# Kernel tuning notes

Measured on AMD Instinct MI355X. Metric: run time of the kernel, lower is better.

The kernel has to match this reference:

```python
import jax, jax.numpy as jnp
import numpy as np

G, P = 128, 32          # num scenes, peds per scene
H, E = 64, 64           # h_dim, embedding_dim_pooling
D1, D2 = 512, 1024      # mlp_pre_pool dims
EPS = 1e-5


def setup_inputs() -> dict:
    key = jax.random.key(0)
    ks = jax.random.split(key, 16)
    N = G * P
    starts = jnp.arange(G, dtype=jnp.int64) * P
    seq_start_end = jnp.stack([starts, starts + P], axis=1)
    def lin(k, fin, fout):
        kw, kb = jax.random.split(k)
        s = 1.0 / np.sqrt(fin)
        return (jax.random.uniform(kw, (fin, fout), jnp.float32, -s, s),
                jax.random.uniform(kb, (fout,), jnp.float32, -s, s))
    Ws, bs = lin(ks[0], 2, E)
    Wv, bv = lin(ks[1], 1, E)
    W1, b1 = lin(ks[2], 3 * E, D1)
    W2, b2 = lin(ks[3], D1, D2)
    return {
        "h_states": jax.random.normal(ks[4], (N, H), jnp.float32),
        "seq_start_end": seq_start_end,
        "end_pos": jax.random.normal(ks[5], (N, 2), jnp.float32),
        "end_pos_speed": jax.random.uniform(ks[6], (N, 1), jnp.float32),
        "Ws": Ws, "bs": bs, "Wv": Wv, "bv": bv,
        "W1": W1, "b1": b1, "g1": jnp.ones((D1,), jnp.float32), "be1": jnp.zeros((D1,), jnp.float32),
        "W2": W2, "b2": b2, "g2": jnp.ones((D2,), jnp.float32), "be2": jnp.zeros((D2,), jnp.float32),
    }


def _bn(h, gamma, beta):
    # BatchNorm1d in train mode, stats over the per-group edge batch (axes 1,2)
    m = h.mean(axis=(1, 2), keepdims=True)
    v = ((h - m) ** 2).mean(axis=(1, 2), keepdims=True)  # biased variance
    return (h - m) * jax.lax.rsqrt(v + EPS) * gamma + beta


def reference(h_states, seq_start_end, end_pos, end_pos_speed,
              Ws, bs, Wv, bv, W1, b1, g1, be1, W2, b2, g2, be2):
    g = seq_start_end.shape[0]
    p = h_states.shape[0] // g
    pos = end_pos.reshape(g, p, 2)
    spd = end_pos_speed.reshape(g, p, 1)
    hid = h_states.reshape(g, p, H)
    # edge (i, j): rel = pos[j] - pos[i]; features of j for hidden & speed
    rel = pos[:, None, :, :] - pos[:, :, None, :]          # [G,P(i),P(j),2]
    rel_e = rel @ Ws + bs                                   # [G,P,P,E]
    spd_e = spd @ Wv + bv                                   # [G,P,E]
    hid_b = jnp.broadcast_to(hid[:, None, :, :], (g, p, p, H))
    spd_b = jnp.broadcast_to(spd_e[:, None, :, :], (g, p, p, E))
    x = jnp.concatenate([rel_e, hid_b, spd_b], axis=-1)     # [G,P,P,3E]
    h1 = jax.nn.relu(_bn(x @ W1 + b1, g1, be1))             # [G,P,P,512]
    h2 = jax.nn.relu(_bn(h1 @ W2 + b2, g2, be2))            # [G,P,P,1024]
    pooled = h2.max(axis=2)                                 # max over j
    return pooled.reshape(g * p, -1)
```

## Files before the change

### kernel.cpp

```cpp
#include <hip/hip_runtime.h>
#include <cstdint>

typedef unsigned short ushort_t;
typedef __attribute__((ext_vector_type(8))) __bf16 bf16x8;
typedef __attribute__((ext_vector_type(4))) float f32x4;
typedef __attribute__((ext_vector_type(4))) int i32x4;

#define NG 128
#define NP 32
#define NH 64
#define ND1 512
#define ND2 1024

__device__ inline ushort_t f2bf(float f) {
    uint32_t u = __float_as_uint(f);
    uint32_t r = (u + 0x7FFFu + ((u >> 16) & 1u)) >> 16;
    return (ushort_t)r;
}

#define GLL16(gp, lp) __builtin_amdgcn_global_load_lds( \
    (const __attribute__((address_space(1))) unsigned int*)(gp), \
    (__attribute__((address_space(3))) unsigned int*)(lp), 16, 0, 0)

__global__ void k2_all(const float* __restrict__ hstates, const float* __restrict__ pos,
                       const float* __restrict__ spd, const float* __restrict__ W1,
                       const float* __restrict__ g1, const float* __restrict__ be1,
                       const float* __restrict__ Ws, const float* __restrict__ bs,
                       const float* __restrict__ Wv, const float* __restrict__ bv,
                       const float* __restrict__ b1, const float* __restrict__ W2,
                       ushort_t* __restrict__ W2T,
                       float* __restrict__ u1, float* __restrict__ w1,
                       float* __restrict__ psum) {
    __shared__ float hid_s[32][64];
    __shared__ float pos_s[32][2];
    __shared__ float spd_s[32];
    __shared__ ushort_t tile[64][65];
    int b = blockIdx.x, tid = threadIdx.x;
    if (b < 256) {
        int t0 = b * 256 + tid;
        #pragma unroll
        for (int z = 0; z < 4; z++) psum[t0 + z * 65536] = 0.f;
        int g = b >> 1;
        int ch = ((b & 1) << 8) + tid;
        for (int t = tid; t < 2048; t += 256) hid_s[t >> 6][t & 63] = hstates[g * 2048 + t];
        if (tid < 64) pos_s[tid >> 1][tid & 1] = pos[g * 64 + tid];
        if (tid < 32) spd_s[tid] = spd[g * 32 + tid];
        float m0 = 0.f, m1 = 0.f, uu = 0.f, vv = b1[ch];
        for (int e = 0; e < 64; e++) {
            float w1a = W1[e * ND1 + ch];
            float w1c = W1[(128 + e) * ND1 + ch];
            m0 += Ws[e] * w1a;
            m1 += Ws[64 + e] * w1a;
            uu += Wv[e] * w1c;
            vv += bs[e] * w1a + bv[e] * w1c;
        }
        __syncthreads();
        float cj[32], qj[32];
        #pragma unroll
        for (int j = 0; j < 32; j++) {
            qj[j] = pos_s[j][0] * m0 + pos_s[j][1] * m1;
            cj[j] = vv + spd_s[j] * uu;
        }
        for (int h = 0; h < 64; h++) {
            float w = W1[(64 + h) * ND1 + ch];
            #pragma unroll
            for (int j = 0; j < 32; j++) cj[j] += hid_s[j][h] * w;
        }
        float S1 = 0.f, S2 = 0.f, C1 = 0.f, Cq = 0.f, C2 = 0.f;
        #pragma unroll
        for (int j = 0; j < 32; j++) {
            S1 += qj[j]; S2 += qj[j] * qj[j];
            C1 += cj[j]; Cq += cj[j] * qj[j]; C2 += cj[j] * cj[j];
        }
        float mean = C1 * (1.0f / 32.0f);
        float sumsq = 64.f * S2 - 2.f * S1 * S1 + 64.f * Cq - 2.f * S1 * C1 + 32.f * C2;
        float var = sumsq * (1.0f / 1024.0f) - mean * mean;
        float A1 = rsqrtf(var + 1e-5f) * g1[ch];
        float B1 = be1[ch] - mean * A1;
        #pragma unroll
        for (int j = 0; j < 32; j++) {
            u1[(g * 32 + j) * ND1 + ch] = (qj[j] + cj[j]) * A1 + B1;
            w1[(g * 32 + j) * ND1 + ch] = qj[j] * A1;
        }
    } else {
        int tb = b - 256;
        int kb2 = tb & 7, nb = tb >> 3;
        #pragma unroll
        for (int e = 0; e < 16; e++) {
            int lin = tid + e * 256;
            int k = lin >> 6, n = lin & 63;
            tile[k][n] = f2bf(W2[(kb2 * 64 + k) * ND2 + nb * 64 + n]);
        }
        __syncthreads();
        #pragma unroll
        for (int e = 0; e < 16; e++) {
            int lin = tid + e * 256;
            int kl = lin & 63, nl = lin >> 6;
            int n = nb * 64 + nl, k = kb2 * 64 + kl;
            int idx = n * ND1 + ((k >> 6) << 6) + (((((k >> 3) & 7) ^ (n & 7))) << 3) + (k & 7);
            W2T[idx] = tile[kl][nl];
        }
    }
}

__global__ void k2b_h1(const float* __restrict__ u1c, const float* __restrict__ w1c,
                       ushort_t* __restrict__ h1) {
    int t = blockIdx.x * 256 + threadIdx.x;
    int k8 = t & 63;
    int row = t >> 6;
    int gc = row >> 10, rem = row & 1023;
    int i = rem >> 5, j = rem & 31;
    const float4* pu = reinterpret_cast<const float4*>(u1c + (size_t)(gc * 32 + j) * ND1 + k8 * 8);
    const float4* pw = reinterpret_cast<const float4*>(w1c + (size_t)(gc * 32 + i) * ND1 + k8 * 8);
    float4 ua = pu[0], ub = pu[1], wa = pw[0], wb = pw[1];
    uint32_t p0 = (uint32_t)f2bf(fmaxf(ua.x - wa.x, 0.f)) | ((uint32_t)f2bf(fmaxf(ua.y - wa.y, 0.f)) << 16);
    uint32_t p1 = (uint32_t)f2bf(fmaxf(ua.z - wa.z, 0.f)) | ((uint32_t)f2bf(fmaxf(ua.w - wa.w, 0.f)) << 16);
    uint32_t p2 = (uint32_t)f2bf(fmaxf(ub.x - wb.x, 0.f)) | ((uint32_t)f2bf(fmaxf(ub.y - wb.y, 0.f)) << 16);
    uint32_t p3 = (uint32_t)f2bf(fmaxf(ub.z - wb.z, 0.f)) | ((uint32_t)f2bf(fmaxf(ub.w - wb.w, 0.f)) << 16);
    i32x4 v = {(int)p0, (int)p1, (int)p2, (int)p3};
    int kt = k8 >> 3, c = k8 & 7;
    *reinterpret_cast<i32x4*>(h1 + (size_t)row * ND1 + (kt << 6) + (((c ^ (row & 7))) << 3)) = v;
}

#define BARX() do { __builtin_amdgcn_sched_barrier(0); __builtin_amdgcn_s_barrier(); __builtin_amdgcn_sched_barrier(0); } while (0)
#define STG(XG, XL, kt, h) do { \
    const char* _g = (XG) + (size_t)(h) * 131072 + (size_t)(kt) * 128; \
    char* _l = (XL) + (((kt) & 1) << 15) + ((h) << 14) + ldsw; \
    GLL16(_g, _l); \
    GLL16(_g + 65536, _l + 8192); \
} while (0)

__global__ __launch_bounds__(512, 2) void k3_gemm(
        const ushort_t* __restrict__ h1, const ushort_t* __restrict__ W2T,
        float* __restrict__ maxv, float* __restrict__ minv,
        float* __restrict__ psum, float* __restrict__ psq, int g0, int nwg8) {
    __shared__ __align__(16) char lds[131072];
    int b = blockIdx.x;
    int orig = (b & 7) * nwg8 + (b >> 3);
    int mt = orig >> 2, nt = orig & 3;
    int tid = threadIdx.x;
    int w = tid >> 6, l = tid & 63;
    int wm = w >> 2, wn = w & 3;
    int lo = l & 15, lhi = l >> 4;

    int srow = w * 8 + (l >> 3);
    int sbyte = (l & 7) * 16;
    const char* Agb = reinterpret_cast<const char*>(h1) + (size_t)(mt * 256 + srow) * 1024 + sbyte;
    const char* Bgb = reinterpret_cast<const char*>(W2T) + (size_t)(nt * 256 + srow) * 1024 + sbyte;
    char* ldsA = lds;
    char* ldsB = lds + 65536;
    int ldsw = w * 1024;

    int csw0 = ((lhi) ^ (lo & 7)) << 4;
    int csw1 = ((4 + lhi) ^ (lo & 7)) << 4;
    const char* aRB = ldsA + wm * 16384 + lo * 128;
    const char* bRB = ldsB + (wn >> 1) * 16384 + ((wn & 1) * 64 + lo) * 128;

    f32x4 acc[8][4];
    #pragma unroll
    for (int x = 0; x < 8; x++)
        #pragma unroll
        for (int y = 0; y < 4; y++) acc[x][y] = (f32x4){0.f, 0.f, 0.f, 0.f};

    bf16x8 a0[4][2], a1[4][2], bb0[2][2], bb1[2][2];

    auto rdA = [&](bf16x8 (&ar)[4][2], int slot, int qm) {
        #pragma unroll
        for (int f = 0; f < 4; f++) {
            ar[f][0] = *reinterpret_cast<const bf16x8*>(aRB + slot * 32768 + (qm * 64 + f * 16) * 128 + csw0);
            ar[f][1] = *reinterpret_cast<const bf16x8*>(aRB + slot * 32768 + (qm * 64 + f * 16) * 128 + csw1);
        }
    };
    auto rdB = [&](bf16x8 (&br)[2][2], int slot, int qn) {
        #pragma unroll
        for (int f = 0; f < 2; f++) {
            br[f][0] = *reinterpret_cast<const bf16x8*>(bRB + slot * 32768 + (qn * 2 + f) * 2048 + csw0);
            br[f][1] = *reinterpret_cast<const bf16x8*>(bRB + slot * 32768 + (qn * 2 + f) * 2048 + csw1);
        }
    };
    auto mm = [&](int fr0, int fc0, bf16x8 (&ar)[4][2], bf16x8 (&br)[2][2]) {
        __builtin_amdgcn_s_setprio(1);
        #pragma unroll
        for (int kc = 0; kc < 2; kc++)
            #pragma unroll
            for (int f = 0; f < 4; f++)
                #pragma unroll
                for (int c = 0; c < 2; c++)
                    acc[fr0 + f][fc0 + c] = __builtin_amdgcn_mfma_f32_16x16x32_bf16(
                        ar[f][kc], br[c][kc], acc[fr0 + f][fc0 + c], 0, 0, 0);
        __builtin_amdgcn_s_setprio(0);
    };

    STG(Agb, ldsA, 0, 0); STG(Agb, ldsA, 0, 1);
    STG(Bgb, ldsB, 0, 0); STG(Bgb, ldsB, 0, 1);
    STG(Agb, ldsA, 1, 0); STG(Agb, ldsA, 1, 1);
    STG(Bgb, ldsB, 1, 0); STG(Bgb, ldsB, 1, 1);
    asm volatile("s_waitcnt vmcnt(8)" ::: "memory");
    BARX();

    for (int J = 0; J < 4; J++) {
        int kB1 = 2 * J + 1;
        rdA(a0, 0, 0); rdB(bb0, 0, 0);
        if (J > 0) STG(Agb, ldsA, kB1, 0);
        BARX();
        mm(0, 0, a0, bb0);
        BARX();
        rdB(bb1, 0, 1);
        if (J > 0) STG(Agb, ldsA, kB1, 1);
        BARX();
        mm(0, 2, a0, bb1);
        BARX();
        rdA(a1, 0, 1);
        if (J < 3) STG(Bgb, ldsB, kB1 + 1, 0);
        BARX();
        mm(4, 0, a1, bb0);
        BARX();
        if (J < 3) STG(Bgb, ldsB, kB1 + 1, 1);
        BARX();
        mm(4, 2, a1, bb1);
        if (J < 3) asm volatile("s_waitcnt vmcnt(4)" ::: "memory");
        else       asm volatile("s_waitcnt vmcnt(0)" ::: "memory");
        BARX();
        rdA(a0, 1, 0); rdB(bb0, 1, 0);
        if (J < 3) STG(Agb, ldsA, kB1 + 1, 0);
        BARX();
        mm(0, 0, a0, bb0);
        BARX();
        rdB(bb1, 1, 1);
        if (J < 3) STG(Agb, ldsA, kB1 + 1, 1);
        BARX();
        mm(0, 2, a0, bb1);
        BARX();
        rdA(a1, 1, 1);
        if (J < 3) STG(Bgb, ldsB, kB1 + 2, 0);
        BARX();
        mm(4, 0, a1, bb0);
        BARX();
        if (J < 3) STG(Bgb, ldsB, kB1 + 2, 1);
        BARX();
        mm(4, 2, a1, bb1);
        if (J < 3) asm volatile("s_waitcnt vmcnt(4)" ::: "memory");
        BARX();
    }

    int g = g0 + (mt >> 2);
    int qq = mt & 3;
    #pragma unroll
    for (int fc = 0; fc < 4; fc++) {
        int col = nt * 256 + wn * 64 + fc * 16 + lo;
        float sm = 0.f, sq = 0.f;
        float mx[4], mn[4];
        #pragma unroll
        for (int m = 0; m < 4; m++) {
            float vmx = -1e30f, vmn = 1e30f;
            #pragma unroll
            for (int fh = 0; fh < 2; fh++)
                #pragma unroll
                for (int r = 0; r < 4; r++) {
                    float y = acc[2 * m + fh][fc][r];
                    vmx = fmaxf(vmx, y); vmn = fminf(vmn, y);
                    sm += y; sq += y * y;
                }
            vmx = fmaxf(vmx, __shfl_xor(vmx, 16, 64));
            vmx = fmaxf(vmx, __shfl_xor(vmx, 32, 64));
            vmn = fminf(vmn, __shfl_xor(vmn, 16, 64));
            vmn = fminf(vmn, __shfl_xor(vmn, 32, 64));
            mx[m] = vmx; mn[m] = vmn;
        }
        sm += __shfl_xor(sm, 16, 64); sm += __shfl_xor(sm, 32, 64);
        sq += __shfl_xor(sq, 16, 64); sq += __shfl_xor(sq, 32, 64);
        if (lhi == 0) {
            #pragma unroll
            for (int m = 0; m < 4; m++) {
                int i = qq * 8 + wm * 4 + m;
                size_t idx = (size_t)(g * 32 + i) * ND2 + col;
                maxv[idx] = mx[m]; minv[idx] = mn[m];
            }
            atomicAdd(&psum[g * ND2 + col], sm);
            atomicAdd(&psq[g * ND2 + col], sq);
        }
    }
}

__global__ void k4_final(const float* __restrict__ maxv, const float* __restrict__ minv,
                         const float* __restrict__ psum, const float* __restrict__ psq,
                         const float* __restrict__ b2, const float* __restrict__ g2,
                         const float* __restrict__ be2, float* __restrict__ out) {
    int g = blockIdx.x >> 2;
    int col = ((blockIdx.x & 3) << 8) + threadIdx.x;
    float b2v = b2[col];
    float s = psum[g * ND2 + col] * (1.f / 1024.f);
    float q = psq[g * ND2 + col] * (1.f / 1024.f);
    float mean = s + b2v;
    float var = q + 2.f * b2v * s + b2v * b2v - mean * mean;
    float A2 = rsqrtf(var + 1e-5f) * g2[col];
    float B2 = be2[col] - mean * A2;
    for (int i = 0; i < 32; i++) {
        size_t idx = (size_t)(g * 32 + i) * ND2 + col;
        float y = ((A2 >= 0.f) ? maxv[idx] : minv[idx]) + b2v;
        out[idx] = fmaxf(y * A2 + B2, 0.f);
    }
}

extern "C" void kernel_launch(void* const* d_in, const int* in_sizes, int n_in,
                              void* d_out, int out_size, void* d_ws, size_t ws_size,
                              hipStream_t stream) {
    (void)in_sizes; (void)n_in; (void)out_size;
    const float* h_states = (const float*)d_in[0];
    const float* end_pos  = (const float*)d_in[2];
    const float* end_spd  = (const float*)d_in[3];
    const float* Ws  = (const float*)d_in[4];
    const float* bs  = (const float*)d_in[5];
    const float* Wv  = (const float*)d_in[6];
    const float* bv  = (const float*)d_in[7];
    const float* W1  = (const float*)d_in[8];
    const float* b1  = (const float*)d_in[9];
    const float* g1  = (const float*)d_in[10];
    const float* be1 = (const float*)d_in[11];
    const float* W2  = (const float*)d_in[12];
    const float* b2  = (const float*)d_in[13];
    const float* g2  = (const float*)d_in[14];
    const float* be2 = (const float*)d_in[15];
    float* ws = (float*)d_ws;
    float* u1   = ws + 2048;
    float* w1x  = ws + 2099200;
    ushort_t* W2T = (ushort_t*)(ws + 4196352);
    float* maxv = ws + 4458496;
    float* minv = ws + 8652800;
    float* psum = ws + 12847104;
    float* psq  = ws + 12978176;
    ushort_t* h1 = (ushort_t*)(ws + 13109248);
    float* out = (float*)d_out;

    const size_t fixed_f = 13109248ULL;
    int CG = 128;
    while (CG > 4 && (fixed_f + (size_t)CG * 262144ULL) * 4ULL > ws_size) CG >>= 1;
    int nch = 128 / CG;

    hipLaunchKernelGGL(k2_all, dim3(384), dim3(256), 0, stream,
                       h_states, end_pos, end_spd, W1, g1, be1,
                       Ws, bs, Wv, bv, b1, W2, W2T, u1, w1x, psum);
    for (int c = 0; c < nch; c++) {
        const float* u1c = u1 + (size_t)c * CG * 32 * ND1;
        const float* w1c = w1x + (size_t)c * CG * 32 * ND1;
        hipLaunchKernelGGL(k2b_h1, dim3(CG * 256), dim3(256), 0, stream, u1c, w1c, h1);
        hipLaunchKernelGGL(k3_gemm, dim3(CG * 16), dim3(512), 0, stream,
                           h1, W2T, maxv, minv, psum, psq, c * CG, CG * 2);
    }
    hipLaunchKernelGGL(k4_final, dim3(512), dim3(256), 0, stream,
                       maxv, minv, psum, psq, b2, g2, be2, out);
}
```

Measured before the change: 306.3 us.

## Fuse h1 materialization into the layer-1 stats kernel

Adds a fused kernel that computes the per-channel layer-1 batchnorm coefficients and writes the bf16 h1 tile directly through a swizzled LDS staging buffer. This removes the separate k2b_h1 kernel and the float u1/w1 intermediate round trip through global memory. When the workspace is large enough it then runs one full-size GEMM launch. The cost is fewer blocks (256) doing the full h1 write, so less parallelism for that phase. It also adds a 32KB LDS stage per block.

```diff
diff --git a/kernel.cpp b/kernel.cpp
--- a/kernel.cpp
+++ b/kernel.cpp
@@ -21,6 +21,114 @@
 #define GLL16(gp, lp) __builtin_amdgcn_global_load_lds( \
     (const __attribute__((address_space(1))) unsigned int*)(gp), \
     (__attribute__((address_space(3))) unsigned int*)(lp), 16, 0, 0)
+
+__global__ void k2_fused(const float* __restrict__ hstates, const float* __restrict__ pos,
+                         const float* __restrict__ spd, const float* __restrict__ W1,
+                         const float* __restrict__ g1, const float* __restrict__ be1,
+                         const float* __restrict__ Ws, const float* __restrict__ bs,
+                         const float* __restrict__ Wv, const float* __restrict__ bv,
+                         const float* __restrict__ b1, const float* __restrict__ W2,
+                         ushort_t* __restrict__ W2T, ushort_t* __restrict__ h1,
+                         float* __restrict__ psum) {
+    __shared__ float hid_s[32][64];
+    __shared__ float pos_s[32][2];
+    __shared__ float spd_s[32];
+    __shared__ ushort_t tile[64][65];
+    __shared__ __align__(16) char stage[32768];
+    int b = blockIdx.x, tid = threadIdx.x;
+    if (b < 256) {
+        int t0 = b * 256 + tid;
+        #pragma unroll
+        for (int z = 0; z < 4; z++) psum[t0 + z * 65536] = 0.f;
+        int g = b >> 1, half = b & 1;
+        int ch = (half << 8) + tid;
+        for (int t = tid; t < 2048; t += 256) hid_s[t >> 6][t & 63] = hstates[g * 2048 + t];
+        if (tid < 64) pos_s[tid >> 1][tid & 1] = pos[g * 64 + tid];
+        if (tid < 32) spd_s[tid] = spd[g * 32 + tid];
+        float m0 = 0.f, m1 = 0.f, uu = 0.f, vv = b1[ch];
+        for (int e = 0; e < 64; e++) {
+            float w1a = W1[e * ND1 + ch];
+            float w1c = W1[(128 + e) * ND1 + ch];
+            m0 += Ws[e] * w1a;
+            m1 += Ws[64 + e] * w1a;
+            uu += Wv[e] * w1c;
+            vv += bs[e] * w1a + bv[e] * w1c;
+        }
+        __syncthreads();
+        float cj[32], qj[32];
+        #pragma unroll
+        for (int j = 0; j < 32; j++) {
+            qj[j] = pos_s[j][0] * m0 + pos_s[j][1] * m1;
+            cj[j] = vv + spd_s[j] * uu;
+        }
+        for (int h = 0; h < 64; h++) {
+            float w = W1[(64 + h) * ND1 + ch];
+            #pragma unroll
+            for (int j = 0; j < 32; j++) cj[j] += hid_s[j][h] * w;
+        }
+        float S1 = 0.f, S2 = 0.f, C1 = 0.f, Cq = 0.f, C2 = 0.f;
+        #pragma unroll
+        for (int j = 0; j < 32; j++) {
+            S1 += qj[j]; S2 += qj[j] * qj[j];
+            C1 += cj[j]; Cq += cj[j] * qj[j]; C2 += cj[j] * cj[j];
+        }
+        float mean = C1 * (1.0f / 32.0f);
+        float sumsq = 64.f * S2 - 2.f * S1 * S1 + 64.f * Cq - 2.f * S1 * C1 + 32.f * C2;
+        float var = sumsq * (1.0f / 1024.0f) - mean * mean;
+        float A1 = rsqrtf(var + 1e-5f) * g1[ch];
+        float B1 = be1[ch] - mean * A1;
+        float uj[32], wi[32];
+        #pragma unroll
+        for (int j = 0; j < 32; j++) {
+            uj[j] = (qj[j] + cj[j]) * A1 + B1;
+            wi[j] = qj[j] * A1;
+        }
+        int wloc = (ch >> 6) & 3;
+        int chsw = (ch >> 3) & 7;
+        int chlo = (ch & 7) * 2;
+        char* sbase = stage + wloc * 128 + chlo;
+        #pragma unroll
+        for (int ib = 0; ib < 16; ib++) {
+            __syncthreads();
+            #pragma unroll
+            for (int ii = 0; ii < 2; ii++) {
+                float w = wi[ib * 2 + ii];
+                #pragma unroll
+                for (int j = 0; j < 32; j++) {
+                    float v = fmaxf(uj[j] - w, 0.f);
+                    *(ushort_t*)(sbase + (ii * 32 + j) * 512 + ((chsw ^ (j & 7)) << 4)) = f2bf(v);
+                }
+            }
+            __syncthreads();
+            int r = tid >> 2, seg = tid & 3;
+            char* gdst = (char*)h1 + (size_t)(g * 1024 + ib * 64 + r) * 1024 + half * 512 + seg * 128;
+            const char* lsrc = stage + r * 512 + seg * 128;
+            #pragma unroll
+            for (int q = 0; q < 8; q++) {
+                int c = ((q ^ (r & 7)) << 4);
+                *reinterpret_cast<i32x4*>(gdst + c) = *reinterpret_cast<const i32x4*>(lsrc + c);
+            }
+        }
+    } else {
+        int tb = b - 256;
+        int kb2 = tb & 7, nb = tb >> 3;
+        #pragma unroll
+        for (int e = 0; e < 16; e++) {
+            int lin = tid + e * 256;
+            int k = lin >> 6, n = lin & 63;
+            tile[k][n] = f2bf(W2[(kb2 * 64 + k) * ND2 + nb * 64 + n]);
+        }
+        __syncthreads();
+        #pragma unroll
+        for (int e = 0; e < 16; e++) {
+            int lin = tid + e * 256;
+            int kl = lin & 63, nl = lin >> 6;
+            int n = nb * 64 + nl, k = kb2 * 64 + kl;
+            int idx = n * ND1 + ((k >> 6) << 6) + (((((k >> 3) & 7) ^ (n & 7))) << 3) + (k & 7);
+            W2T[idx] = tile[kl][nl];
+        }
+    }
+}
 
 __global__ void k2_all(const float* __restrict__ hstates, const float* __restrict__ pos,
                        const float* __restrict__ spd, const float* __restrict__ W1,
@@ -333,19 +441,28 @@
     float* out = (float*)d_out;
 
     const size_t fixed_f = 13109248ULL;
-    int CG = 128;
-    while (CG > 4 && (fixed_f + (size_t)CG * 262144ULL) * 4ULL > ws_size) CG >>= 1;
-    int nch = 128 / CG;
-
-    hipLaunchKernelGGL(k2_all, dim3(384), dim3(256), 0, stream,
-                       h_states, end_pos, end_spd, W1, g1, be1,
-                       Ws, bs, Wv, bv, b1, W2, W2T, u1, w1x, psum);
-    for (int c = 0; c < nch; c++) {
-        const float* u1c = u1 + (size_t)c * CG * 32 * ND1;
-        const float* w1c = w1x + (size_t)c * CG * 32 * ND1;
-        hipLaunchKernelGGL(k2b_h1, dim3(CG * 256), dim3(256), 0, stream, u1c, w1c, h1);
-        hipLaunchKernelGGL(k3_gemm, dim3(CG * 16), dim3(512), 0, stream,
-                           h1, W2T, maxv, minv, psum, psq, c * CG, CG * 2);
+    const size_t need_full = (fixed_f + 128ULL * 262144ULL) * 4ULL;
+
+    if (ws_size >= need_full) {
+        hipLaunchKernelGGL(k2_fused, dim3(384), dim3(256), 0, stream,
+                           h_states, end_pos, end_spd, W1, g1, be1,
+                           Ws, bs, Wv, bv, b1, W2, W2T, h1, psum);
+        hipLaunchKernelGGL(k3_gemm, dim3(2048), dim3(512), 0, stream,
+                           h1, W2T, maxv, minv, psum, psq, 0, 256);
+    } else {
+        int CG = 128;
+        while (CG > 4 && (fixed_f + (size_t)CG * 262144ULL) * 4ULL > ws_size) CG >>= 1;
+        int nch = 128 / CG;
+        hipLaunchKernelGGL(k2_all, dim3(384), dim3(256), 0, stream,
+                           h_states, end_pos, end_spd, W1, g1, be1,
+                           Ws, bs, Wv, bv, b1, W2, W2T, u1, w1x, psum);
+        for (int c = 0; c < nch; c++) {
+            const float* u1c = u1 + (size_t)c * CG * 32 * ND1;
+            const float* w1c = w1x + (size_t)c * CG * 32 * ND1;
+            hipLaunchKernelGGL(k2b_h1, dim3(CG * 256), dim3(256), 0, stream, u1c, w1c, h1);
+            hipLaunchKernelGGL(k3_gemm, dim3(CG * 16), dim3(512), 0, stream,
+                               h1, W2T, maxv, minv, psum, psq, c * CG, CG * 2);
+        }
     }
     hipLaunchKernelGGL(k4_final, dim3(512), dim3(256), 0, stream,
                        maxv, minv, psum, psq, b2, g2, be2, out);
```

Measured after the change: 320.5 us. +4.7%, slower.
